# Performance work log

Measured on AMD Instinct MI355X. Metric: run time of the kernel, lower is better.

Reference implementation:

```python
import jax, jax.numpy as jnp
import numpy as np

D_MODEL = 1024
N_HEADS = 16
D_H = D_MODEL // N_HEADS
B, S = 2, 2048


def setup_inputs() -> dict:
    key = jax.random.key(0)
    ks = jax.random.split(key, 12)
    s = 1.0 / np.sqrt(D_MODEL)
    inp = {
        "Q": jax.random.normal(ks[0], (B, S, D_MODEL), jnp.float32),
        "K": jax.random.normal(ks[1], (B, S, D_MODEL), jnp.float32),
        "V": jax.random.normal(ks[2], (B, S, D_MODEL), jnp.float32),
        # causal mask: True means masked out (matches masked_fill semantics)
        "masked": jnp.broadcast_to(~jnp.tril(jnp.ones((S, S), bool)), (B, S, S)),
        "WQ_w": jax.random.uniform(ks[3], (D_MODEL, D_MODEL), jnp.float32, -s, s),
        "WQ_b": jax.random.uniform(ks[4], (D_MODEL,), jnp.float32, -s, s),
        "WK_w": jax.random.uniform(ks[5], (D_MODEL, D_MODEL), jnp.float32, -s, s),
        "WK_b": jax.random.uniform(ks[6], (D_MODEL,), jnp.float32, -s, s),
        "WV_w": jax.random.uniform(ks[7], (D_MODEL, D_MODEL), jnp.float32, -s, s),
        "WV_b": jax.random.uniform(ks[8], (D_MODEL,), jnp.float32, -s, s),
        "Wo_w": jax.random.uniform(ks[9], (D_MODEL, D_MODEL), jnp.float32, -s, s),
        "Wo_b": jax.random.uniform(ks[10], (D_MODEL,), jnp.float32, -s, s),
    }
    return inp


def reference(Q, K, V, masked, WQ_w, WQ_b, WK_w, WK_b, WV_w, WV_b, Wo_w, Wo_b):
    b = Q.shape[0]
    # torch Linear: y = x @ W^T + b
    def split_heads(x):
        return x.reshape(b, -1, N_HEADS, D_H).transpose(0, 2, 1, 3)  # [B,H,S,d_h]

    q = split_heads(Q @ WQ_w.T + WQ_b)
    k = split_heads(K @ WK_w.T + WK_b)
    v = split_heads(V @ WV_w.T + WV_b)

    scores = jnp.einsum("bhqd,bhkd->bhqk", q, k) / np.sqrt(D_H)
    scores = jnp.where(masked[:, None, :, :], jnp.float32(-1e9), scores)
    attn = jax.nn.softmax(scores, axis=-1)
    ctx = jnp.einsum("bhqk,bhkd->bhqd", attn, v)  # [B,H,S,d_h]
    ctx = ctx.transpose(0, 2, 1, 3).reshape(b, -1, N_HEADS * D_H)
    return ctx @ Wo_w.T + Wo_b
```

## Files before the change

kernel.cpp:

```cpp
#include <hip/hip_runtime.h>
#include <hip/hip_bf16.h>
#include <math.h>


typedef __bf16 bf16_t;
typedef bf16_t bf16x8 __attribute__((ext_vector_type(8)));
typedef bf16_t bf16x4 __attribute__((ext_vector_type(4)));
typedef float f32x4 __attribute__((ext_vector_type(4)));

#define MFMA16(a, b, c) __builtin_amdgcn_mfma_f32_16x16x32_bf16(a, b, c, 0, 0, 0)

constexpr int S_LEN = 2048;
constexpr int DMODEL = 1024;
constexpr int DHEAD = 64;
constexpr int MTOT = 2 * S_LEN;
constexpr size_t NQ = (size_t)MTOT * DMODEL;
constexpr size_t NW = (size_t)DMODEL * DMODEL;
constexpr float ESC = 0.18033688011112042f;

__device__ __forceinline__ void load_lds16(const void* g, void* l) {
  __builtin_amdgcn_global_load_lds((const __attribute__((address_space(1))) void*)g,
                                   (__attribute__((address_space(3))) void*)l, 16, 0, 0);
}

__device__ __forceinline__ void swap32(unsigned& a, unsigned& b) {
#if __has_builtin(__builtin_amdgcn_permlane32_swap)
  auto r = __builtin_amdgcn_permlane32_swap(a, b, false, false);
  a = r[0]; b = r[1];
#else
  asm volatile("s_nop 1\n\tv_permlane32_swap_b32 %0, %1\n\ts_nop 1"
               : "+v"(a), "+v"(b));
#endif
}
__device__ __forceinline__ void swap16(unsigned& a, unsigned& b) {
#if __has_builtin(__builtin_amdgcn_permlane16_swap)
  auto r = __builtin_amdgcn_permlane16_swap(a, b, false, false);
  a = r[0]; b = r[1];
#else
  asm volatile("s_nop 1\n\tv_permlane16_swap_b32 %0, %1\n\ts_nop 1"
               : "+v"(a), "+v"(b));
#endif
}

__device__ __forceinline__ float fexp2(float x) {
#if __has_builtin(__builtin_amdgcn_exp2f)
  return __builtin_amdgcn_exp2f(x);
#else
  float r;
  asm("v_exp_f32 %0, %1\n\ts_nop 1" : "=v"(r) : "v"(x));
  return r;
#endif
}

__global__ __launch_bounds__(256) void convert_all(
    const float* __restrict__ Q, const float* __restrict__ K, const float* __restrict__ V,
    const float* __restrict__ W0, const float* __restrict__ W1, const float* __restrict__ W2,
    const float* __restrict__ W3, bf16_t* __restrict__ dst) {
  const size_t i = ((size_t)blockIdx.x * 256 + threadIdx.x) * 4;
  const float* s;
  size_t off = i;
  if (off < NQ) { s = Q; }
  else if (off < 2 * NQ) { s = K; off -= NQ; }
  else if (off < 3 * NQ) { s = V; off -= 2 * NQ; }
  else {
    off -= 3 * NQ;
    if (off < NW) { s = W0; }
    else if (off < 2 * NW) { s = W1; off -= NW; }
    else if (off < 3 * NW) { s = W2; off -= 2 * NW; }
    else { s = W3; off -= 3 * NW; }
  }
  const float4 v4 = *(const float4*)(s + off);
  bf16x4 b;
  b[0] = (bf16_t)v4.x; b[1] = (bf16_t)v4.y; b[2] = (bf16_t)v4.z; b[3] = (bf16_t)v4.w;
  *(bf16x4*)(dst + i) = b;
}

template <int BK>
__device__ __forceinline__ void gemm_loop(const bf16_t* __restrict__ Ab,
                                          const bf16_t* __restrict__ Wb,
                                          bf16_t* As, bf16_t* Ws,
                                          f32x4 (&acc)[4][4], int wave, int lane) {
  constexpr int CH = BK / 8;
  constexpr int RPI = 64 / CH;
  constexpr int IPW = BK / 16;
  const int col = lane & 15, quad = lane >> 4;
  const int wm = (wave >> 1) * 64, wn = (wave & 1) * 64;
  const int srow = lane / CH;
  const int sch = lane % CH;

  for (int k0 = 0; k0 < 1024; k0 += BK) {
    __syncthreads();
#pragma unroll
    for (int i = 0; i < IPW; i++) {
      const int rbase = (i * 4 + wave) * RPI;
      const int g = sch ^ ((rbase + srow) & 7);
      load_lds16(Ab + (size_t)(rbase + srow) * 1024 + k0 + g * 8, As + rbase * BK);
      load_lds16(Wb + (size_t)(rbase + srow) * 1024 + k0 + g * 8, Ws + rbase * BK);
    }
    __syncthreads();
#pragma unroll
    for (int kc = 0; kc < BK / 32; kc++) {
      const int slot = (kc * 4 + quad) ^ (col & 7);
      bf16x8 af[4], wf[4];
#pragma unroll
      for (int i = 0; i < 4; i++) af[i] = *(const bf16x8*)&As[(wm + i * 16 + col) * BK + slot * 8];
#pragma unroll
      for (int j = 0; j < 4; j++) wf[j] = *(const bf16x8*)&Ws[(wn + j * 16 + col) * BK + slot * 8];
#pragma unroll
      for (int i = 0; i < 4; i++)
#pragma unroll
        for (int j = 0; j < 4; j++) acc[i][j] = MFMA16(af[i], wf[j], acc[i][j]);
    }
  }
}

__global__ __launch_bounds__(256, 3) void gemm_qkv(const bf16_t* __restrict__ Abase,
                                                   const bf16_t* __restrict__ Wbase,
                                                   const float* __restrict__ b0,
                                                   const float* __restrict__ b1,
                                                   const float* __restrict__ b2,
                                                   bf16_t* __restrict__ obase) {
  __shared__ bf16_t As[128 * 64];
  __shared__ bf16_t Ws[128 * 64];
  const int z = blockIdx.z;
  const int bm = blockIdx.x * 128, bn = blockIdx.y * 128;
  const int lane = threadIdx.x & 63, wave = threadIdx.x >> 6;
  const int col = lane & 15, quad = lane >> 4;
  const int wm = (wave >> 1) * 64, wn = (wave & 1) * 64;

  f32x4 acc[4][4];
#pragma unroll
  for (int i = 0; i < 4; i++)
#pragma unroll
    for (int j = 0; j < 4; j++)
#pragma unroll
      for (int r = 0; r < 4; r++) acc[i][j][r] = 0.f;

  const bf16_t* A = Abase + z * NQ + (size_t)bm * 1024;
  const bf16_t* W = Wbase + z * NW + (size_t)bn * 1024;
  const float* bias = (z == 0) ? b0 : ((z == 1) ? b1 : b2);
  bf16_t* out = obase + z * NQ;

  gemm_loop<64>(A, W, As, Ws, acc, wave, lane);

  const float esc = (z == 0) ? ESC : 1.0f;
#pragma unroll
  for (int i = 0; i < 4; i++) {
#pragma unroll
    for (int j = 0; j < 4; j++) {
      const int n = bn + wn + j * 16 + col;
      const float bv = bias[n];
      const int h = n >> 6, dh = n & 63;
      if (z < 2) {
#pragma unroll
        for (int r = 0; r < 4; r++) {
          const int m = bm + wm + i * 16 + quad * 4 + r;
          const int b = m >> 11, s = m & 2047;
          out[((size_t)((b * 16 + h) * S_LEN + s) << 6) | dh] =
              (bf16_t)((acc[i][j][r] + bv) * esc);
        }
      } else {
        const int m0 = bm + wm + i * 16 + quad * 4;
        const int b = m0 >> 11, s0 = m0 & 2047;
        bf16x4 p4;
#pragma unroll
        for (int r = 0; r < 4; r++) p4[r] = (bf16_t)(acc[i][j][r] + bv);
        *(bf16x4*)&out[(((size_t)((b * 16 + h) * DHEAD + dh)) << 11) | s0] = p4;
      }
    }
  }
}

__global__ __launch_bounds__(256, 2) void gemm_out(const bf16_t* __restrict__ A,
                                                   const bf16_t* __restrict__ W,
                                                   const float* __restrict__ bias,
                                                   float* __restrict__ out) {
  __shared__ bf16_t As[64 * 64];
  __shared__ bf16_t Ws[128 * 64];
  const int bm = blockIdx.x * 64, bn = blockIdx.y * 128;
  const int lane = threadIdx.x & 63, wave = threadIdx.x >> 6;
  const int col = lane & 15, quad = lane >> 4;
  const int wm = (wave >> 1) * 32, wn = (wave & 1) * 64;

  f32x4 acc[2][4];
#pragma unroll
  for (int i = 0; i < 2; i++)
#pragma unroll
    for (int j = 0; j < 4; j++)
#pragma unroll
      for (int r = 0; r < 4; r++) acc[i][j][r] = 0.f;

  const int srow = lane >> 3, s7 = lane & 7;
  const bf16_t* Ab = A + (size_t)bm * 1024;
  const bf16_t* Wb = W + (size_t)bn * 1024;

  for (int k0 = 0; k0 < 1024; k0 += 64) {
    __syncthreads();
#pragma unroll
    for (int i = 0; i < 2; i++) {
      const int rbase = (i * 4 + wave) * 8;
      const int g = s7 ^ srow;
      load_lds16(Ab + (size_t)(rbase + srow) * 1024 + k0 + g * 8, As + rbase * 64);
    }
#pragma unroll
    for (int i = 0; i < 4; i++) {
      const int rbase = (i * 4 + wave) * 8;
      const int g = s7 ^ srow;
      load_lds16(Wb + (size_t)(rbase + srow) * 1024 + k0 + g * 8, Ws + rbase * 64);
    }
    __syncthreads();
#pragma unroll
    for (int kc = 0; kc < 2; kc++) {
      const int slot = (kc * 4 + quad) ^ (col & 7);
      bf16x8 af[2], wf[4];
#pragma unroll
      for (int i = 0; i < 2; i++) af[i] = *(const bf16x8*)&As[(wm + i * 16 + col) * 64 + slot * 8];
#pragma unroll
      for (int j = 0; j < 4; j++) wf[j] = *(const bf16x8*)&Ws[(wn + j * 16 + col) * 64 + slot * 8];
#pragma unroll
      for (int i = 0; i < 2; i++)
#pragma unroll
        for (int j = 0; j < 4; j++) acc[i][j] = MFMA16(af[i], wf[j], acc[i][j]);
    }
  }

#pragma unroll
  for (int i = 0; i < 2; i++)
#pragma unroll
    for (int j = 0; j < 4; j++) {
      const int n = bn + wn + j * 16 + col;
      const float bv = bias[n];
#pragma unroll
      for (int r = 0; r < 4; r++) {
        const int m = bm + wm + i * 16 + quad * 4 + r;
        out[(size_t)m * DMODEL + n] = acc[i][j][r] + bv;
      }
    }
}

__global__ __launch_bounds__(256, 2) void attn(const bf16_t* __restrict__ q,
                                               const bf16_t* __restrict__ k,
                                               const bf16_t* __restrict__ vT,
                                               bf16_t* __restrict__ ctx,
                                               float* __restrict__ pO,
                                               float* __restrict__ pL) {
  const int bh = blockIdx.x;
  const int p = blockIdx.y;
  const int s = blockIdx.z;
  const int tB = 15 - p;
  const int nA = s ? 0 : (2 * p + 2);
  const int cB0 = s ? (15 - 2 * p) : 0;
  const int lane = threadIdx.x & 63, wave = threadIdx.x >> 6;
  const int col = lane & 15, quad = lane >> 4;
  const int qrel = wave * 16 + col;

  __shared__ bf16_t Ks[2][64 * 64];
  __shared__ bf16_t Vs[2][64 * 64];

  const bf16_t* kbh = k + (size_t)bh * S_LEN * DHEAD;
  const bf16_t* vbh = vT + (size_t)bh * DHEAD * S_LEN;

  const int srow8 = lane >> 3, s7 = lane & 7;
  const int g8 = s7 ^ srow8;

  auto stage = [&](int c, int b) {
#pragma unroll
    for (int i = 0; i < 2; i++) {
      const int rbase = (i * 4 + wave) * 8;
      load_lds16(kbh + (size_t)(c * 64 + rbase + srow8) * DHEAD + g8 * 8,
                 &Ks[b][rbase * 64]);
    }
#pragma unroll
    for (int i = 0; i < 2; i++) {
      const int dbase = (i * 4 + wave) * 8;
      load_lds16(vbh + (size_t)(dbase + srow8) * S_LEN + c * 64 + g8 * 8,
                 &Vs[b][dbase * 64]);
    }
  };

  bf16x8 aqw[2][2];
  f32x4 o0[4], o1[4], lacc0, lacc1;
  const f32x4 Zv = {0.f, 0.f, 0.f, 0.f};

  auto expw = [&](const f32x4& sv, int nb, bool dmask, f32x4& lac,
                  unsigned& w0, unsigned& w1) {
    union { bf16x4 v; unsigned u[2]; } pw;
#pragma unroll
    for (int r = 0; r < 4; r++) {
      float pv = fexp2(sv[r]);
      if (dmask && (nb * 16 + quad * 4 + r) > qrel) pv = 0.f;
      lac[r] += pv;
      pw.v[r] = (bf16_t)pv;
    }
    w0 = pw.u[0]; w1 = pw.u[1];
  };

  stage(cB0, 0);
  int buf = 0;

#pragma unroll 1
  for (int i = 0; i < 17; ++i) {
    const bool inB = (i >= nA);
    const int c = inB ? (cB0 + i - nA) : i;
    const int cm = inB ? (2 * tB + 1) : (2 * p + 1);

    if (i == 0 || i == nA) {
      const int tq = inB ? tB : p;
      const bf16_t* qb = q + ((size_t)bh * S_LEN + tq * 128 + qrel) * DHEAD;
      aqw[0][0] = *(const bf16x8*)(qb + quad * 8);
      aqw[0][1] = *(const bf16x8*)(qb + 32 + quad * 8);
      aqw[1][0] = *(const bf16x8*)(qb + (size_t)64 * DHEAD + quad * 8);
      aqw[1][1] = *(const bf16x8*)(qb + (size_t)64 * DHEAD + 32 + quad * 8);
#pragma unroll
      for (int r = 0; r < 4; r++) { lacc0[r] = 0.f; lacc1[r] = 0.f; }
#pragma unroll
      for (int db = 0; db < 4; db++)
#pragma unroll
        for (int r = 0; r < 4; r++) { o0[db][r] = 0.f; o1[db][r] = 0.f; }
    }

    __syncthreads();

    if (i < 16) {
      const int i1 = i + 1;
      const int c1 = (i1 < nA) ? i1 : (cB0 + i1 - nA);
      stage(c1, buf ^ 1);
    }

    const bool skip0 = (c == cm);
    const bool mask0 = (c == cm - 1);
    const bool mask1 = (c == cm);

    f32x4 s0[4], s1[4];
    {
      const int sl = quad ^ (col & 7);
      bf16x8 kf[4];
#pragma unroll
      for (int nb = 0; nb < 4; nb++)
        kf[nb] = *(const bf16x8*)&Ks[buf][(nb * 16 + col) * 64 + sl * 8];
      __builtin_amdgcn_s_setprio(1);
      if (!skip0) {
#pragma unroll
        for (int nb = 0; nb < 4; nb++) s0[nb] = MFMA16(kf[nb], aqw[0][0], Zv);
      }
#pragma unroll
      for (int nb = 0; nb < 4; nb++) s1[nb] = MFMA16(kf[nb], aqw[1][0], Zv);
      __builtin_amdgcn_s_setprio(0);
    }
    {
      const int sl = (4 + quad) ^ (col & 7);
      bf16x8 kf[4];
#pragma unroll
      for (int nb = 0; nb < 4; nb++)
        kf[nb] = *(const bf16x8*)&Ks[buf][(nb * 16 + col) * 64 + sl * 8];
      __builtin_amdgcn_s_setprio(1);
      if (!skip0) {
#pragma unroll
        for (int nb = 0; nb < 4; nb++) s0[nb] = MFMA16(kf[nb], aqw[0][1], s0[nb]);
      }
#pragma unroll
      for (int nb = 0; nb < 4; nb++) s1[nb] = MFMA16(kf[nb], aqw[1][1], s1[nb]);
      __builtin_amdgcn_s_setprio(0);
    }

#pragma unroll
    for (int kcp = 0; kcp < 2; kcp++) {
      const int sl = (kcp * 4 + quad) ^ (col & 7);
      bf16x8 bv[4];
#pragma unroll
      for (int db = 0; db < 4; db++)
        bv[db] = *(const bf16x8*)&Vs[buf][(db * 16 + col) * 64 + sl * 8];

      union { unsigned u[4]; bf16x8 v; } pa1, pa0;
      {
        unsigned X0, X1, Y0, Y1;
        expw(s1[2 * kcp], 2 * kcp, mask1, lacc1, X0, X1);
        expw(s1[2 * kcp + 1], 2 * kcp + 1, mask1, lacc1, Y0, Y1);
        swap32(X0, Y0); swap16(X0, Y0);
        swap32(X1, Y1); swap16(X1, Y1);
        pa1.u[0] = X0; pa1.u[1] = X1; pa1.u[2] = Y0; pa1.u[3] = Y1;
      }
      if (!skip0) {
        unsigned X0, X1, Y0, Y1;
        expw(s0[2 * kcp], 2 * kcp, mask0, lacc0, X0, X1);
        expw(s0[2 * kcp + 1], 2 * kcp + 1, mask0, lacc0, Y0, Y1);
        swap32(X0, Y0); swap16(X0, Y0);
        swap32(X1, Y1); swap16(X1, Y1);
        pa0.u[0] = X0; pa0.u[1] = X1; pa0.u[2] = Y0; pa0.u[3] = Y1;
      }
      __builtin_amdgcn_s_setprio(1);
      if (!skip0) {
#pragma unroll
        for (int db = 0; db < 4; db++) o0[db] = MFMA16(bv[db], pa0.v, o0[db]);
      }
#pragma unroll
      for (int db = 0; db < 4; db++) o1[db] = MFMA16(bv[db], pa1.v, o1[db]);
      __builtin_amdgcn_s_setprio(0);
    }

    if (i == nA - 1) {
      float l0 = lacc0[0] + lacc0[1] + lacc0[2] + lacc0[3];
      l0 += __shfl_xor(l0, 16); l0 += __shfl_xor(l0, 32);
      float l1 = lacc1[0] + lacc1[1] + lacc1[2] + lacc1[3];
      l1 += __shfl_xor(l1, 16); l1 += __shfl_xor(l1, 32);
      const float inv0 = 1.f / l0, inv1 = 1.f / l1;
      const int b = bh >> 4, h = bh & 15;
      bf16_t* cb0 = ctx + ((size_t)(b * S_LEN + p * 128 + qrel)) * DMODEL + h * DHEAD;
      bf16_t* cb1 = cb0 + (size_t)64 * DMODEL;
#pragma unroll
      for (int db = 0; db < 4; db++) {
        bf16x4 w0, w1;
#pragma unroll
        for (int r = 0; r < 4; r++) {
          w0[r] = (bf16_t)(o0[db][r] * inv0);
          w1[r] = (bf16_t)(o1[db][r] * inv1);
        }
        *(bf16x4*)&cb0[db * 16 + quad * 4] = w0;
        *(bf16x4*)&cb1[db * 16 + quad * 4] = w1;
      }
    }
    buf ^= 1;
  }

  float l0 = lacc0[0] + lacc0[1] + lacc0[2] + lacc0[3];
  l0 += __shfl_xor(l0, 16); l0 += __shfl_xor(l0, 32);
  float l1 = lacc1[0] + lacc1[1] + lacc1[2] + lacc1[3];
  l1 += __shfl_xor(l1, 16); l1 += __shfl_xor(l1, 32);
  const int slot = ((bh * 8 + p) << 1) | s;
  float* myO = pO + (size_t)slot * (128 * 64);
  float* myL = pL + slot * 128;
#pragma unroll
  for (int db = 0; db < 4; db++) {
    *(f32x4*)&myO[(size_t)qrel * 64 + db * 16 + quad * 4] = o0[db];
    *(f32x4*)&myO[(size_t)(64 + qrel) * 64 + db * 16 + quad * 4] = o1[db];
  }
  if (quad == 0) { myL[qrel] = l0; myL[64 + qrel] = l1; }
}

__global__ __launch_bounds__(256) void combine(const float* __restrict__ pO,
                                               const float* __restrict__ pL,
                                               bf16_t* __restrict__ ctx) {
  const int pair = blockIdx.x;
  const int bh = pair >> 3, p = pair & 7;
  const int tB = 15 - p;
  const int b = bh >> 4, h = bh & 15;
  const float* O0 = pO + (size_t)(pair * 2 + 0) * (128 * 64);
  const float* O1 = pO + (size_t)(pair * 2 + 1) * (128 * 64);
  const float* L0 = pL + (pair * 2 + 0) * 128;
  const float* L1 = pL + (pair * 2 + 1) * 128;
#pragma unroll
  for (int n = 0; n < 8; n++) {
    const int idx = n * 1024 + threadIdx.x * 4;
    const int r = idx >> 6, cdh = idx & 63;
    const f32x4 a = *(const f32x4*)&O0[idx];
    const f32x4 c4 = *(const f32x4*)&O1[idx];
    const float inv = 1.f / (L0[r] + L1[r]);
    bf16x4 w;
#pragma unroll
    for (int j = 0; j < 4; j++) w[j] = (bf16_t)((a[j] + c4[j]) * inv);
    *(bf16x4*)&ctx[((size_t)(b * S_LEN + tB * 128 + r)) * DMODEL + h * DHEAD + cdh] = w;
  }
}

extern "C" void kernel_launch(void* const* d_in, const int* in_sizes, int n_in,
                              void* d_out, int out_size, void* d_ws, size_t ws_size,
                              hipStream_t stream) {
  const float* Q = (const float*)d_in[0];
  const float* K = (const float*)d_in[1];
  const float* V = (const float*)d_in[2];
  const float* WQw = (const float*)d_in[4];
  const float* WQb = (const float*)d_in[5];
  const float* WKw = (const float*)d_in[6];
  const float* WKb = (const float*)d_in[7];
  const float* WVw = (const float*)d_in[8];
  const float* WVb = (const float*)d_in[9];
  const float* Wow = (const float*)d_in[10];
  const float* Wob = (const float*)d_in[11];

  bf16_t* base = (bf16_t*)d_ws;
  bf16_t* Wc = base + 3 * NQ;
  bf16_t* qp = base + 3 * NQ + 4 * NW;
  bf16_t* ctx = base;
  float* pO = (float*)(base + NQ);
  float* pL = (float*)(base + 3 * NQ);

  const size_t total = 3 * NQ + 4 * NW;
  convert_all<<<dim3((unsigned)(total / 4 / 256)), dim3(256), 0, stream>>>(
      Q, K, V, WQw, WKw, WVw, Wow, base);

  gemm_qkv<<<dim3(32, 8, 3), dim3(256), 0, stream>>>(base, Wc, WQb, WKb, WVb, qp);
  attn<<<dim3(32, 8, 2), dim3(256), 0, stream>>>(qp, qp + NQ, qp + 2 * NQ, ctx, pO, pL);
  combine<<<dim3(256), dim3(256), 0, stream>>>(pO, pL, ctx);
  gemm_out<<<dim3(64, 8), dim3(256), 0, stream>>>(ctx, Wc + 3 * NW, Wob, (float*)d_out);
}
```

Before: 225.5 us.

## Split causal attention work into three equal chunks per tile pair

The attention grid goes from 2 to 3 splits per (head, tile-pair). The 34 KV chunks of each paired query tiles (p and 15-p) are divided into 12/11/11-chunk segments. Every segment writes partial O and L to a new workspace region, and the combine kernel now sums up to three partials for both tiles instead of writing tile p directly. The aim is more blocks with balanced work, plus higher occupancy through launch_bounds 3. The cost is extra partial-result traffic and a combine over 512 blocks.

```diff
diff --git a/kernel.cpp b/kernel.cpp
--- a/kernel.cpp
+++ b/kernel.cpp
@@ -238,18 +238,17 @@
     }
 }
 
-__global__ __launch_bounds__(256, 2) void attn(const bf16_t* __restrict__ q,
+__global__ __launch_bounds__(256, 3) void attn(const bf16_t* __restrict__ q,
                                                const bf16_t* __restrict__ k,
                                                const bf16_t* __restrict__ vT,
-                                               bf16_t* __restrict__ ctx,
                                                float* __restrict__ pO,
                                                float* __restrict__ pL) {
   const int bh = blockIdx.x;
   const int p = blockIdx.y;
   const int s = blockIdx.z;
-  const int tB = 15 - p;
-  const int nA = s ? 0 : (2 * p + 2);
-  const int cB0 = s ? (15 - 2 * p) : 0;
+  const int bnd = 2 * p + 2;
+  const int gs = (s == 0) ? 0 : (s == 1) ? 12 : 23;
+  const int n = (s == 0) ? 12 : 11;
   const int lane = threadIdx.x & 63, wave = threadIdx.x >> 6;
   const int col = lane & 15, quad = lane >> 4;
   const int qrel = wave * 16 + col;
@@ -281,6 +280,37 @@
   bf16x8 aqw[2][2];
   f32x4 o0[4], o1[4], lacc0, lacc1;
   const f32x4 Zv = {0.f, 0.f, 0.f, 0.f};
+
+  auto setup = [&](int tile_) {
+    const int tq = tile_ ? (15 - p) : p;
+    const bf16_t* qb = q + ((size_t)bh * S_LEN + tq * 128 + qrel) * DHEAD;
+    aqw[0][0] = *(const bf16x8*)(qb + quad * 8);
+    aqw[0][1] = *(const bf16x8*)(qb + 32 + quad * 8);
+    aqw[1][0] = *(const bf16x8*)(qb + (size_t)64 * DHEAD + quad * 8);
+    aqw[1][1] = *(const bf16x8*)(qb + (size_t)64 * DHEAD + 32 + quad * 8);
+#pragma unroll
+    for (int r = 0; r < 4; r++) { lacc0[r] = 0.f; lacc1[r] = 0.f; }
+#pragma unroll
+    for (int db = 0; db < 4; db++)
+#pragma unroll
+      for (int r = 0; r < 4; r++) { o0[db][r] = 0.f; o1[db][r] = 0.f; }
+  };
+
+  auto flush = [&](int tileSel) {
+    float l0 = lacc0[0] + lacc0[1] + lacc0[2] + lacc0[3];
+    l0 += __shfl_xor(l0, 16); l0 += __shfl_xor(l0, 32);
+    float l1 = lacc1[0] + lacc1[1] + lacc1[2] + lacc1[3];
+    l1 += __shfl_xor(l1, 16); l1 += __shfl_xor(l1, 32);
+    const int slot = ((bh * 8 + p) * 2 + tileSel) * 3 + s;
+    float* myO = pO + (size_t)slot * (128 * 64);
+    float* myL = pL + slot * 128;
+#pragma unroll
+    for (int db = 0; db < 4; db++) {
+      *(f32x4*)&myO[(size_t)qrel * 64 + db * 16 + quad * 4] = o0[db];
+      *(f32x4*)&myO[(size_t)(64 + qrel) * 64 + db * 16 + quad * 4] = o1[db];
+    }
+    if (quad == 0) { myL[qrel] = l0; myL[64 + qrel] = l1; }
+  };
 
   auto expw = [&](const f32x4& sv, int nb, bool dmask, f32x4& lac,
                   unsigned& w0, unsigned& w1) {
@@ -295,36 +325,24 @@
     w0 = pw.u[0]; w1 = pw.u[1];
   };
 
-  stage(cB0, 0);
+  int tile = (gs < bnd) ? 0 : 1;
+  stage(gs - (tile ? bnd : 0), 0);
   int buf = 0;
 
 #pragma unroll 1
-  for (int i = 0; i < 17; ++i) {
-    const bool inB = (i >= nA);
-    const int c = inB ? (cB0 + i - nA) : i;
-    const int cm = inB ? (2 * tB + 1) : (2 * p + 1);
-
-    if (i == 0 || i == nA) {
-      const int tq = inB ? tB : p;
-      const bf16_t* qb = q + ((size_t)bh * S_LEN + tq * 128 + qrel) * DHEAD;
-      aqw[0][0] = *(const bf16x8*)(qb + quad * 8);
-      aqw[0][1] = *(const bf16x8*)(qb + 32 + quad * 8);
-      aqw[1][0] = *(const bf16x8*)(qb + (size_t)64 * DHEAD + quad * 8);
-      aqw[1][1] = *(const bf16x8*)(qb + (size_t)64 * DHEAD + 32 + quad * 8);
-#pragma unroll
-      for (int r = 0; r < 4; r++) { lacc0[r] = 0.f; lacc1[r] = 0.f; }
-#pragma unroll
-      for (int db = 0; db < 4; db++)
-#pragma unroll
-        for (int r = 0; r < 4; r++) { o0[db][r] = 0.f; o1[db][r] = 0.f; }
-    }
+  for (int i = 0; i < n; ++i) {
+    const int g = gs + i;
+    if (i == 0) setup(tile);
+    else if (g == bnd) { flush(0); tile = 1; setup(1); }
+    const int c = g - (tile ? bnd : 0);
+    const int tq = tile ? (15 - p) : p;
+    const int cm = 2 * tq + 1;
 
     __syncthreads();
 
-    if (i < 16) {
-      const int i1 = i + 1;
-      const int c1 = (i1 < nA) ? i1 : (cB0 + i1 - nA);
-      stage(c1, buf ^ 1);
+    if (i + 1 < n) {
+      const int g1 = g + 1;
+      stage((g1 < bnd) ? g1 : g1 - bnd, buf ^ 1);
     }
 
     const bool skip0 = (c == cm);
@@ -397,68 +415,46 @@
       for (int db = 0; db < 4; db++) o1[db] = MFMA16(bv[db], pa1.v, o1[db]);
       __builtin_amdgcn_s_setprio(0);
     }
-
-    if (i == nA - 1) {
-      float l0 = lacc0[0] + lacc0[1] + lacc0[2] + lacc0[3];
-      l0 += __shfl_xor(l0, 16); l0 += __shfl_xor(l0, 32);
-      float l1 = lacc1[0] + lacc1[1] + lacc1[2] + lacc1[3];
-      l1 += __shfl_xor(l1, 16); l1 += __shfl_xor(l1, 32);
-      const float inv0 = 1.f / l0, inv1 = 1.f / l1;
-      const int b = bh >> 4, h = bh & 15;
-      bf16_t* cb0 = ctx + ((size_t)(b * S_LEN + p * 128 + qrel)) * DMODEL + h * DHEAD;
-      bf16_t* cb1 = cb0 + (size_t)64 * DMODEL;
-#pragma unroll
-      for (int db = 0; db < 4; db++) {
-        bf16x4 w0, w1;
-#pragma unroll
-        for (int r = 0; r < 4; r++) {
-          w0[r] = (bf16_t)(o0[db][r] * inv0);
-          w1[r] = (bf16_t)(o1[db][r] * inv1);
-        }
-        *(bf16x4*)&cb0[db * 16 + quad * 4] = w0;
-        *(bf16x4*)&cb1[db * 16 + quad * 4] = w1;
-      }
-    }
     buf ^= 1;
   }
 
-  float l0 = lacc0[0] + lacc0[1] + lacc0[2] + lacc0[3];
-  l0 += __shfl_xor(l0, 16); l0 += __shfl_xor(l0, 32);
-  float l1 = lacc1[0] + lacc1[1] + lacc1[2] + lacc1[3];
-  l1 += __shfl_xor(l1, 16); l1 += __shfl_xor(l1, 32);
-  const int slot = ((bh * 8 + p) << 1) | s;
-  float* myO = pO + (size_t)slot * (128 * 64);
-  float* myL = pL + slot * 128;
-#pragma unroll
-  for (int db = 0; db < 4; db++) {
-    *(f32x4*)&myO[(size_t)qrel * 64 + db * 16 + quad * 4] = o0[db];
-    *(f32x4*)&myO[(size_t)(64 + qrel) * 64 + db * 16 + quad * 4] = o1[db];
-  }
-  if (quad == 0) { myL[qrel] = l0; myL[64 + qrel] = l1; }
+  flush(tile);
 }
 
 __global__ __launch_bounds__(256) void combine(const float* __restrict__ pO,
                                                const float* __restrict__ pL,
                                                bf16_t* __restrict__ ctx) {
-  const int pair = blockIdx.x;
-  const int bh = pair >> 3, p = pair & 7;
-  const int tB = 15 - p;
+  const int idx = blockIdx.x;
+  const int bh = idx >> 4;
+  const int p = (idx >> 1) & 7;
+  const int tile = idx & 1;
+  const int bnd = 2 * p + 2;
+  const int tq = tile ? (15 - p) : p;
   const int b = bh >> 4, h = bh & 15;
-  const float* O0 = pO + (size_t)(pair * 2 + 0) * (128 * 64);
-  const float* O1 = pO + (size_t)(pair * 2 + 1) * (128 * 64);
-  const float* L0 = pL + (pair * 2 + 0) * 128;
-  const float* L1 = pL + (pair * 2 + 1) * 128;
-#pragma unroll
-  for (int n = 0; n < 8; n++) {
-    const int idx = n * 1024 + threadIdx.x * 4;
-    const int r = idx >> 6, cdh = idx & 63;
-    const f32x4 a = *(const f32x4*)&O0[idx];
-    const f32x4 c4 = *(const f32x4*)&O1[idx];
-    const float inv = 1.f / (L0[r] + L1[r]);
+  const int sb = ((bh * 8 + p) * 2 + tile) * 3;
+  const int smask = tile ? ((bnd < 12) ? 7 : 6) : ((bnd > 12) ? 3 : 1);
+
+#pragma unroll
+  for (int nblk = 0; nblk < 8; nblk++) {
+    const int e = nblk * 1024 + threadIdx.x * 4;
+    const int r = e >> 6, dh = e & 63;
+    f32x4 acc = {0.f, 0.f, 0.f, 0.f};
+    float L = 0.f;
+#pragma unroll
+    for (int s2 = 0; s2 < 3; s2++) {
+      if ((smask >> s2) & 1) {
+        const float* O = pO + (size_t)(sb + s2) * (128 * 64);
+        const f32x4 v = *(const f32x4*)&O[e];
+#pragma unroll
+        for (int j = 0; j < 4; j++) acc[j] += v[j];
+        L += pL[(sb + s2) * 128 + r];
+      }
+    }
+    const float inv = 1.f / L;
     bf16x4 w;
 #pragma unroll
-    for (int j = 0; j < 4; j++) w[j] = (bf16_t)((a[j] + c4[j]) * inv);
-    *(bf16x4*)&ctx[((size_t)(b * S_LEN + tB * 128 + r)) * DMODEL + h * DHEAD + cdh] = w;
+    for (int j = 0; j < 4; j++) w[j] = (bf16_t)(acc[j] * inv);
+    *(bf16x4*)&ctx[((size_t)(b * S_LEN + tq * 128 + r)) * DMODEL + h * DHEAD + dh] = w;
   }
 }
 
@@ -481,15 +477,15 @@
   bf16_t* Wc = base + 3 * NQ;
   bf16_t* qp = base + 3 * NQ + 4 * NW;
   bf16_t* ctx = base;
-  float* pO = (float*)(base + NQ);
-  float* pL = (float*)(base + 3 * NQ);
+  float* pO = (float*)(base + 6 * NQ + 4 * NW);
+  float* pL = pO + (size_t)1536 * (128 * 64);
 
   const size_t total = 3 * NQ + 4 * NW;
   convert_all<<<dim3((unsigned)(total / 4 / 256)), dim3(256), 0, stream>>>(
       Q, K, V, WQw, WKw, WVw, Wow, base);
 
   gemm_qkv<<<dim3(32, 8, 3), dim3(256), 0, stream>>>(base, Wc, WQb, WKb, WVb, qp);
-  attn<<<dim3(32, 8, 2), dim3(256), 0, stream>>>(qp, qp + NQ, qp + 2 * NQ, ctx, pO, pL);
-  combine<<<dim3(256), dim3(256), 0, stream>>>(pO, pL, ctx);
+  attn<<<dim3(32, 8, 3), dim3(256), 0, stream>>>(qp, qp + NQ, qp + 2 * NQ, pO, pL);
+  combine<<<dim3(512), dim3(256), 0, stream>>>(pO, pL, ctx);
   gemm_out<<<dim3(64, 8), dim3(256), 0, stream>>>(ctx, Wc + 3 * NW, Wob, (float*)d_out);
 }
```

Measured after the change: 235.1 us. 4.3% more time.

## Fuse fp32-to-bf16 activation conversion into the QKV projection GEMM

Applied to the files above, without the earlier changes.

The QKV GEMM now reads fp32 Q/K/V directly. It prefetches the next A tile into registers, converts it to bf16 and writes it into swizzled LDS, while the weights still arrive through direct global-to-LDS loads. The standalone conversion kernel now handles only the weights, which removes a full read and write of all three activation tensors. In exchange the GEMM moves twice the bytes for the A operand, uses more registers for the prefetch, and replaces async LDS loads with register staging. The partial-sum buffer pL is moved into the QKV weight scratch region, and the attention Q-setup code is pulled into a lambda.

```diff
diff --git a/kernel.cpp b/kernel.cpp
--- a/kernel.cpp
+++ b/kernel.cpp
@@ -52,69 +52,26 @@
 #endif
 }
 
-__global__ __launch_bounds__(256) void convert_all(
-    const float* __restrict__ Q, const float* __restrict__ K, const float* __restrict__ V,
-    const float* __restrict__ W0, const float* __restrict__ W1, const float* __restrict__ W2,
-    const float* __restrict__ W3, bf16_t* __restrict__ dst) {
+__global__ __launch_bounds__(256) void convert_w(
+    const float* __restrict__ W0, const float* __restrict__ W1,
+    const float* __restrict__ W2, const float* __restrict__ W3,
+    bf16_t* __restrict__ dst) {
   const size_t i = ((size_t)blockIdx.x * 256 + threadIdx.x) * 4;
   const float* s;
   size_t off = i;
-  if (off < NQ) { s = Q; }
-  else if (off < 2 * NQ) { s = K; off -= NQ; }
-  else if (off < 3 * NQ) { s = V; off -= 2 * NQ; }
-  else {
-    off -= 3 * NQ;
-    if (off < NW) { s = W0; }
-    else if (off < 2 * NW) { s = W1; off -= NW; }
-    else if (off < 3 * NW) { s = W2; off -= 2 * NW; }
-    else { s = W3; off -= 3 * NW; }
-  }
+  if (off < NW) { s = W0; }
+  else if (off < 2 * NW) { s = W1; off -= NW; }
+  else if (off < 3 * NW) { s = W2; off -= 2 * NW; }
+  else { s = W3; off -= 3 * NW; }
   const float4 v4 = *(const float4*)(s + off);
   bf16x4 b;
   b[0] = (bf16_t)v4.x; b[1] = (bf16_t)v4.y; b[2] = (bf16_t)v4.z; b[3] = (bf16_t)v4.w;
   *(bf16x4*)(dst + i) = b;
 }
 
-template <int BK>
-__device__ __forceinline__ void gemm_loop(const bf16_t* __restrict__ Ab,
-                                          const bf16_t* __restrict__ Wb,
-                                          bf16_t* As, bf16_t* Ws,
-                                          f32x4 (&acc)[4][4], int wave, int lane) {
-  constexpr int CH = BK / 8;
-  constexpr int RPI = 64 / CH;
-  constexpr int IPW = BK / 16;
-  const int col = lane & 15, quad = lane >> 4;
-  const int wm = (wave >> 1) * 64, wn = (wave & 1) * 64;
-  const int srow = lane / CH;
-  const int sch = lane % CH;
-
-  for (int k0 = 0; k0 < 1024; k0 += BK) {
-    __syncthreads();
-#pragma unroll
-    for (int i = 0; i < IPW; i++) {
-      const int rbase = (i * 4 + wave) * RPI;
-      const int g = sch ^ ((rbase + srow) & 7);
-      load_lds16(Ab + (size_t)(rbase + srow) * 1024 + k0 + g * 8, As + rbase * BK);
-      load_lds16(Wb + (size_t)(rbase + srow) * 1024 + k0 + g * 8, Ws + rbase * BK);
-    }
-    __syncthreads();
-#pragma unroll
-    for (int kc = 0; kc < BK / 32; kc++) {
-      const int slot = (kc * 4 + quad) ^ (col & 7);
-      bf16x8 af[4], wf[4];
-#pragma unroll
-      for (int i = 0; i < 4; i++) af[i] = *(const bf16x8*)&As[(wm + i * 16 + col) * BK + slot * 8];
-#pragma unroll
-      for (int j = 0; j < 4; j++) wf[j] = *(const bf16x8*)&Ws[(wn + j * 16 + col) * BK + slot * 8];
-#pragma unroll
-      for (int i = 0; i < 4; i++)
-#pragma unroll
-        for (int j = 0; j < 4; j++) acc[i][j] = MFMA16(af[i], wf[j], acc[i][j]);
-    }
-  }
-}
-
-__global__ __launch_bounds__(256, 3) void gemm_qkv(const bf16_t* __restrict__ Abase,
+__global__ __launch_bounds__(256, 3) void gemm_qkv(const float* __restrict__ Qf,
+                                                   const float* __restrict__ Kf,
+                                                   const float* __restrict__ Vf,
                                                    const bf16_t* __restrict__ Wbase,
                                                    const float* __restrict__ b0,
                                                    const float* __restrict__ b1,
@@ -127,6 +84,7 @@
   const int lane = threadIdx.x & 63, wave = threadIdx.x >> 6;
   const int col = lane & 15, quad = lane >> 4;
   const int wm = (wave >> 1) * 64, wn = (wave & 1) * 64;
+  const int srow8 = lane >> 3, g8 = (lane & 7) ^ srow8;
 
   f32x4 acc[4][4];
 #pragma unroll
@@ -136,12 +94,53 @@
 #pragma unroll
       for (int r = 0; r < 4; r++) acc[i][j][r] = 0.f;
 
-  const bf16_t* A = Abase + z * NQ + (size_t)bm * 1024;
-  const bf16_t* W = Wbase + z * NW + (size_t)bn * 1024;
+  const float* Af = ((z == 0) ? Qf : (z == 1) ? Kf : Vf) + (size_t)bm * 1024;
+  const bf16_t* Wb = Wbase + z * NW + (size_t)bn * 1024;
   const float* bias = (z == 0) ? b0 : ((z == 1) ? b1 : b2);
   bf16_t* out = obase + z * NQ;
 
-  gemm_loop<64>(A, W, As, Ws, acc, wave, lane);
+  f32x4 pre[8];
+  auto grloadA = [&](int k0) {
+#pragma unroll
+    for (int i = 0; i < 4; i++) {
+      const int rbase = (i * 4 + wave) * 8;
+      const float* src = Af + (size_t)(rbase + srow8) * 1024 + k0 + g8 * 8;
+      pre[2 * i] = *(const f32x4*)src;
+      pre[2 * i + 1] = *(const f32x4*)(src + 4);
+    }
+  };
+
+  grloadA(0);
+  for (int k0 = 0; k0 < 1024; k0 += 64) {
+    __syncthreads();
+#pragma unroll
+    for (int i = 0; i < 4; i++) {
+      const int rbase = (i * 4 + wave) * 8;
+      bf16x8 pk;
+#pragma unroll
+      for (int j = 0; j < 4; j++) {
+        pk[j] = (bf16_t)pre[2 * i][j];
+        pk[4 + j] = (bf16_t)pre[2 * i + 1][j];
+      }
+      *(bf16x8*)&As[rbase * 64 + lane * 8] = pk;
+      load_lds16(Wb + (size_t)(rbase + srow8) * 1024 + k0 + g8 * 8, Ws + rbase * 64);
+    }
+    __syncthreads();
+    if (k0 + 64 < 1024) grloadA(k0 + 64);
+#pragma unroll
+    for (int kc = 0; kc < 2; kc++) {
+      const int slot = (kc * 4 + quad) ^ (col & 7);
+      bf16x8 af[4], wf[4];
+#pragma unroll
+      for (int i = 0; i < 4; i++) af[i] = *(const bf16x8*)&As[(wm + i * 16 + col) * 64 + slot * 8];
+#pragma unroll
+      for (int j = 0; j < 4; j++) wf[j] = *(const bf16x8*)&Ws[(wn + j * 16 + col) * 64 + slot * 8];
+#pragma unroll
+      for (int i = 0; i < 4; i++)
+#pragma unroll
+        for (int j = 0; j < 4; j++) acc[i][j] = MFMA16(af[i], wf[j], acc[i][j]);
+    }
+  }
 
   const float esc = (z == 0) ? ESC : 1.0f;
 #pragma unroll
@@ -282,6 +281,21 @@
   f32x4 o0[4], o1[4], lacc0, lacc1;
   const f32x4 Zv = {0.f, 0.f, 0.f, 0.f};
 
+  auto setup = [&](int tile_) {
+    const int tq = tile_ ? tB : p;
+    const bf16_t* qb = q + ((size_t)bh * S_LEN + tq * 128 + qrel) * DHEAD;
+    aqw[0][0] = *(const bf16x8*)(qb + quad * 8);
+    aqw[0][1] = *(const bf16x8*)(qb + 32 + quad * 8);
+    aqw[1][0] = *(const bf16x8*)(qb + (size_t)64 * DHEAD + quad * 8);
+    aqw[1][1] = *(const bf16x8*)(qb + (size_t)64 * DHEAD + 32 + quad * 8);
+#pragma unroll
+    for (int r = 0; r < 4; r++) { lacc0[r] = 0.f; lacc1[r] = 0.f; }
+#pragma unroll
+    for (int db = 0; db < 4; db++)
+#pragma unroll
+      for (int r = 0; r < 4; r++) { o0[db][r] = 0.f; o1[db][r] = 0.f; }
+  };
+
   auto expw = [&](const f32x4& sv, int nb, bool dmask, f32x4& lac,
                   unsigned& w0, unsigned& w1) {
     union { bf16x4 v; unsigned u[2]; } pw;
@@ -295,6 +309,7 @@
     w0 = pw.u[0]; w1 = pw.u[1];
   };
 
+  int tile = (0 >= nA) ? 1 : 0;
   stage(cB0, 0);
   int buf = 0;
 
@@ -304,20 +319,8 @@
     const int c = inB ? (cB0 + i - nA) : i;
     const int cm = inB ? (2 * tB + 1) : (2 * p + 1);
 
-    if (i == 0 || i == nA) {
-      const int tq = inB ? tB : p;
-      const bf16_t* qb = q + ((size_t)bh * S_LEN + tq * 128 + qrel) * DHEAD;
-      aqw[0][0] = *(const bf16x8*)(qb + quad * 8);
-      aqw[0][1] = *(const bf16x8*)(qb + 32 + quad * 8);
-      aqw[1][0] = *(const bf16x8*)(qb + (size_t)64 * DHEAD + quad * 8);
-      aqw[1][1] = *(const bf16x8*)(qb + (size_t)64 * DHEAD + 32 + quad * 8);
-#pragma unroll
-      for (int r = 0; r < 4; r++) { lacc0[r] = 0.f; lacc1[r] = 0.f; }
-#pragma unroll
-      for (int db = 0; db < 4; db++)
-#pragma unroll
-        for (int r = 0; r < 4; r++) { o0[db][r] = 0.f; o1[db][r] = 0.f; }
-    }
+    if (i == 0) setup(inB ? 1 : 0);
+    else if (i == nA) setup(1);
 
     __syncthreads();
 
@@ -482,13 +485,13 @@
   bf16_t* qp = base + 3 * NQ + 4 * NW;
   bf16_t* ctx = base;
   float* pO = (float*)(base + NQ);
-  float* pL = (float*)(base + 3 * NQ);
-
-  const size_t total = 3 * NQ + 4 * NW;
-  convert_all<<<dim3((unsigned)(total / 4 / 256)), dim3(256), 0, stream>>>(
-      Q, K, V, WQw, WKw, WVw, Wow, base);
-
-  gemm_qkv<<<dim3(32, 8, 3), dim3(256), 0, stream>>>(base, Wc, WQb, WKb, WVb, qp);
+  float* pL = (float*)(base + (NQ / 2));
+  pL = (float*)(Wc + NW / 2);
+
+  convert_w<<<dim3((unsigned)(4 * NW / 4 / 256)), dim3(256), 0, stream>>>(
+      WQw, WKw, WVw, Wow, Wc);
+
+  gemm_qkv<<<dim3(32, 8, 3), dim3(256), 0, stream>>>(Q, K, V, Wc, WQb, WKb, WVb, qp);
   attn<<<dim3(32, 8, 2), dim3(256), 0, stream>>>(qp, qp + NQ, qp + 2 * NQ, ctx, pO, pL);
   combine<<<dim3(256), dim3(256), 0, stream>>>(pO, pL, ctx);
   gemm_out<<<dim3(64, 8), dim3(256), 0, stream>>>(ctx, Wc + 3 * NW, Wob, (float*)d_out);
```

Result: no change. 224.6 us (-0.4%).
